# Performance work log

Hardware: AMD Instinct MI355X
Metric: run time of the kernel (lower is better)

## Reference

```python
import jax, jax.numpy as jnp
import numpy as np

NEG_SLOPE = 0.2  # PyG GATConv default negative_slope


def _gat_conv(h, src, dst, N, W, a_src, a_dst, b, heads):
    """PyG GATConv (eval mode, self-loops already in src/dst).
    h: [N, F_in], W: [F_in, heads*C], a_src/a_dst: [heads, C], b: [heads*C]."""
    C = W.shape[1] // heads
    hl = (h @ W).reshape(N, heads, C)                      # [N,H,C]
    al_s = jnp.einsum('nhc,hc->nh', hl, a_src)             # [N,H]
    al_d = jnp.einsum('nhc,hc->nh', hl, a_dst)             # [N,H]
    e = jax.nn.leaky_relu(al_s[src] + al_d[dst], NEG_SLOPE)  # [E,H]
    # segment softmax over incoming edges of each destination node
    m = jax.ops.segment_max(e, dst, num_segments=N)        # [N,H]
    ex = jnp.exp(e - m[dst])
    s = jax.ops.segment_sum(ex, dst, num_segments=N)
    alpha = ex / (s[dst] + 1e-16)                          # [E,H]
    out = jax.ops.segment_sum(hl[src] * alpha[:, :, None], dst, num_segments=N)
    return out.reshape(N, heads * C) + b


def setup_inputs() -> dict:
    key = jax.random.key(0)
    ks = jax.random.split(key, 16)
    N, E, D = 30000, 240000, 64
    NUM_ENT, NUM_REL, NUM_DRUGS = 100000, 64, 200
    sc = 0.1
    return {
        'x': jax.random.randint(ks[0], (N,), 0, NUM_ENT),
        'edge_index': jax.random.randint(ks[1], (2, E), 0, N),
        'edge_type': jax.random.randint(ks[2], (N,), 0, NUM_REL),
        'ent_emb': jax.random.normal(ks[3], (NUM_ENT, D), jnp.float32) * sc,
        'rel_emb': jax.random.normal(ks[4], (NUM_REL, D), jnp.float32) * sc,
        'W1': jax.random.normal(ks[5], (2 * D, 8 * D), jnp.float32) * sc,
        'att1_src': jax.random.normal(ks[6], (8, D), jnp.float32) * sc,
        'att1_dst': jax.random.normal(ks[7], (8, D), jnp.float32) * sc,
        'b1': jax.random.normal(ks[8], (8 * D,), jnp.float32) * sc,
        'W2': jax.random.normal(ks[9], (9 * D, D), jnp.float32) * sc,
        'att2_src': jax.random.normal(ks[10], (1, D), jnp.float32) * sc,
        'att2_dst': jax.random.normal(ks[11], (1, D), jnp.float32) * sc,
        'b2': jax.random.normal(ks[12], (D,), jnp.float32) * sc,
        'fc_w': jax.random.normal(ks[13], (D, NUM_DRUGS), jnp.float32) * sc,
        'fc_b': jax.random.normal(ks[14], (NUM_DRUGS,), jnp.float32) * sc,
    }


def reference(x, edge_index, edge_type, ent_emb, rel_emb, W1, att1_src, att1_dst, b1,
              W2, att2_src, att2_dst, b2, fc_w, fc_b):
    N = x.shape[0]
    loop = jnp.arange(N)
    src = jnp.concatenate([edge_index[0], loop])  # GATConv add_self_loops=True
    dst = jnp.concatenate([edge_index[1], loop])
    ent = ent_emb[x]                               # [N,D]
    rel = rel_emb[edge_type]                       # [N,D]
    h = jnp.concatenate([ent, rel], axis=-1)       # [N,2D]  (dropout is identity in eval)
    h = jax.nn.elu(_gat_conv(h, src, dst, N, W1, att1_src, att1_dst, b1, heads=8))  # [N,8D]
    h = jnp.concatenate([h, ent], axis=-1)         # [N,9D]
    h = jax.nn.elu(_gat_conv(h, src, dst, N, W2, att2_src, att2_dst, b2, heads=1))  # [N,D]
    g = jnp.mean(h, axis=0, keepdims=True)         # [1,D]
    return g @ fc_w + fc_b                         # [1,num_drugs]
```

## Files before the change

### kernel.cpp

```cpp
#include <hip/hip_runtime.h>
#include <math.h>

#define NEG_SLOPE 0.2f

typedef __attribute__((ext_vector_type(8))) short short8;
typedef __attribute__((ext_vector_type(4))) float f32x4;
typedef __attribute__((ext_vector_type(2))) float f32x2;

__device__ __forceinline__ float lrelu(float v) { return v > 0.f ? v : NEG_SLOPE * v; }
__device__ __forceinline__ float elu(float v) { return v > 0.f ? v : (__expf(v) - 1.f); }
__device__ __forceinline__ unsigned short f2b(float f) {
    unsigned u = __float_as_uint(f);
    return (unsigned short)((u + 0x7FFFu + ((u >> 16) & 1u)) >> 16);
}
__device__ __forceinline__ float blo(unsigned v) { return __uint_as_float(v << 16); }
__device__ __forceinline__ float bhi(unsigned v) { return __uint_as_float(v & 0xFFFF0000u); }
__device__ __forceinline__ unsigned packb(float a, float b) {
    return ((unsigned)f2b(b) << 16) | (unsigned)f2b(a);
}
__device__ __forceinline__ unsigned short pack8(float a, float b) {
    return (unsigned short)(__builtin_amdgcn_cvt_pk_fp8_f32(a, b, 0, false) & 0xFFFF);
}
__device__ __forceinline__ f32x2 unpack8(unsigned v) {
    return __builtin_amdgcn_cvt_pk_f32_fp8((int)v, false);
}
__device__ __forceinline__ f32x2 unpack8hi(unsigned v) {
    return __builtin_amdgcn_cvt_pk_f32_fp8((int)v, true);
}
__device__ __forceinline__ unsigned bpack_trunc(f32x2 f) {
    return (__float_as_uint(f.y) & 0xFFFF0000u) | (__float_as_uint(f.x) >> 16);
}
__device__ __forceinline__ int sw(int r, int o) { return (o ^ (r & 7)) << 3; }

__global__ __launch_bounds__(256) void init_k(int* __restrict__ zbase, int zwords,
                                              const float* __restrict__ W1,
                                              const float* __restrict__ W2,
                                              const float* __restrict__ a1s,
                                              const float* __restrict__ a1d,
                                              unsigned short* __restrict__ wsb,
                                              unsigned short* __restrict__ W1t,
                                              unsigned short* __restrict__ W2t) {
    int t = blockIdx.x * blockDim.x + threadIdx.x;
    int stride = gridDim.x * blockDim.x;
    for (int i = t; i < zwords; i += stride) zbase[i] = 0;
    for (int i = t; i < 2048; i += stride) {
        int hh = i >> 7, k = i & 127, h = hh & 7;
        const float* aw = (hh < 8) ? a1s : a1d;
        const float* wr = W1 + (size_t)k * 512 + h * 64;
        float s_ = 0.f;
#pragma unroll 16
        for (int c = 0; c < 64; c++) s_ += wr[c] * aw[h * 64 + c];
        wsb[i] = f2b(s_);
    }
    for (int i = t; i < 512 * 128; i += stride) {
        int n = i >> 7, kk = i & 127;
        W1t[i] = f2b(W1[(size_t)kk * 512 + n]);
    }
    for (int i = t; i < 64 * 576; i += stride) {
        int n = i / 576, k = i % 576;
        W2t[i] = f2b(W2[(size_t)k * 64 + n]);
    }
}

__global__ void prep_k(const int* __restrict__ x, const int* __restrict__ et,
                       const int* __restrict__ ei,
                       const float* __restrict__ ent_emb, const float* __restrict__ rel_emb,
                       unsigned* __restrict__ h1b2, unsigned short* __restrict__ h1q,
                       int* __restrict__ deg, int N, int E) {
    int t = blockIdx.x * blockDim.x + threadIdx.x;
    if (t < N * 64) {
        int n = t >> 6, j = t & 63;
        float v0, v1;
        if (j < 32) {
            const float* e = ent_emb + (size_t)x[n] * 64 + 2 * j;
            v0 = e[0]; v1 = e[1];
        } else {
            const float* r = rel_emb + (size_t)et[n] * 64 + 2 * (j - 32);
            v0 = r[0]; v1 = r[1];
        }
        h1b2[t] = packb(v0, v1);
        h1q[t] = pack8(v0, v1);
    }
    if (t < E + N) {
        int dst = t < E ? ei[E + t] : t - E;
        atomicAdd(&deg[dst], 1);
    }
}

__global__ __launch_bounds__(256) void attn1_k(const unsigned short* __restrict__ A,
                                               const unsigned short* __restrict__ Bt,
                                               float* __restrict__ als, float* __restrict__ ald,
                                               int M) {
    __shared__ __align__(16) unsigned short As[128 * 128];
    __shared__ __align__(16) unsigned short Bs[16 * 128];
    int tid = threadIdx.x;
    int m0 = blockIdx.x * 128;
    for (int c = tid; c < 2048; c += 256) {
        int r = c >> 4, o = c & 15;
        int gr = m0 + r;
        uint4 v = make_uint4(0u, 0u, 0u, 0u);
        if (gr < M) v = *(const uint4*)(A + (size_t)gr * 128 + o * 8);
        *(uint4*)(As + r * 128 + sw(r, o)) = v;
    }
    if (tid < 256) {
        int r = tid >> 4, o = tid & 15;
        uint4 v = *(const uint4*)(Bt + (size_t)r * 128 + o * 8);
        *(uint4*)(Bs + r * 128 + sw(r, o)) = v;
    }
    __syncthreads();
    int w = tid >> 6, lane = tid & 63;
    int wr = w * 32;
    int m16 = lane & 15, quad = lane >> 4;
    f32x4 acc[2] = {};
#pragma unroll
    for (int kk = 0; kk < 128; kk += 32) {
        int ob = (kk >> 3) + quad;
        short8 b = *(const short8*)(Bs + m16 * 128 + sw(m16, ob));
#pragma unroll
        for (int i = 0; i < 2; i++) {
            int r = wr + i * 16 + m16;
            short8 a = *(const short8*)(As + r * 128 + sw(r, ob));
            acc[i] = __builtin_amdgcn_mfma_f32_16x16x32_bf16(a, b, acc[i], 0, 0, 0);
        }
    }
#pragma unroll
    for (int i = 0; i < 2; i++)
#pragma unroll
        for (int reg = 0; reg < 4; reg++) {
            int row = m0 + wr + i * 16 + quad * 4 + reg;
            if (row < M) {
                if (m16 < 8) als[row * 8 + m16] = acc[i][reg];
                else         ald[row * 8 + (m16 - 8)] = acc[i][reg];
            }
        }
}

__global__ __launch_bounds__(256) void scan_k(const int* __restrict__ deg,
                                              int* __restrict__ offs,
                                              int* __restrict__ bstate,
                                              int N, int Etot, int NB) {
    __shared__ int s[256];
    __shared__ int sbase;
    int b = blockIdx.x, t = threadIdx.x;
    int i = b * 256 + t;
    int v = (i < N) ? deg[i] : 0;
    s[t] = v;
    __syncthreads();
    for (int off = 1; off < 256; off <<= 1) {
        int tmp = (t >= off) ? s[t - off] : 0;
        __syncthreads();
        s[t] += tmp;
        __syncthreads();
    }
    int total = s[255];
    if (t == 0) {
        if (b == 0) {
            atomicExch(&bstate[0], (total << 2) | 2);
            sbase = 0;
        } else {
            atomicExch(&bstate[b], (total << 2) | 1);
            int run = 0;
            for (int p = b - 1; p >= 0;) {
                int stv;
                do { stv = atomicAdd(&bstate[p], 0); } while ((stv & 3) == 0);
                run += (stv >> 2);
                if ((stv & 3) == 2) break;
                p--;
            }
            atomicExch(&bstate[b], ((run + total) << 2) | 2);
            sbase = run;
        }
    }
    __syncthreads();
    if (i < N) offs[i] = sbase + s[t] - v;
    if (b == NB - 1 && t == 0) offs[N] = Etot;
}

__global__ void fill_k(const int* __restrict__ ei, int E, int N,
                       const int* __restrict__ offs, int* __restrict__ cursor,
                       int* __restrict__ csr) {
    int e = blockIdx.x * blockDim.x + threadIdx.x;
    if (e >= E + N) return;
    int src = e < E ? ei[e] : e - E;
    int dst = e < E ? ei[E + e] : e - E;
    int pos = offs[dst] + atomicAdd(&cursor[dst], 1);
    csr[pos] = src;
}

__global__ __launch_bounds__(256) void alpha1_k(const float* __restrict__ als1,
                                                const float* __restrict__ ald1,
                                                const int* __restrict__ offs,
                                                const int* __restrict__ csr,
                                                float* __restrict__ ex1,
                                                float* __restrict__ inv1, int N) {
    int slot = threadIdx.x >> 3, h = threadIdx.x & 7;
    int n = blockIdx.x * 32 + slot;
    if (n >= N) return;
    float dl = ald1[n * 8 + h];
    int p0 = offs[n], p1 = offs[n + 1];
    float ssum = 0.f;
    for (int p = p0; p < p1; p++) {
        int src = csr[p];
        float xv = __expf(lrelu(als1[src * 8 + h] + dl));
        ex1[(size_t)p * 8 + h] = xv;
        ssum += xv;
    }
    inv1[n * 8 + h] = 8.f / (ssum + 1e-16f);
}

__global__ __launch_bounds__(256) void aggG_k(const unsigned short* __restrict__ h1q,
                                              const unsigned* __restrict__ h1b2,
                                              const float* __restrict__ ex1,
                                              const float* __restrict__ inv1,
                                              const int* __restrict__ offs,
                                              const int* __restrict__ csr,
                                              unsigned short* __restrict__ Gq,
                                              unsigned* __restrict__ h2u, int N) {
    int wv = threadIdx.x >> 6;
    int t = threadIdx.x & 63;
    int n = blockIdx.x * 4 + wv;
    if (n >= N) return;
    int p0 = offs[n], p1 = offs[n + 1];
    float a0[8] = {}, a1[8] = {};
    int p = p0;
    for (; p + 1 < p1; p += 2) {
        int sA = csr[p], sB = csr[p + 1];
        float4 eA0 = *(const float4*)(ex1 + (size_t)p * 8);
        float4 eA1 = *(const float4*)(ex1 + (size_t)p * 8 + 4);
        float4 eB0 = *(const float4*)(ex1 + (size_t)p * 8 + 8);
        float4 eB1 = *(const float4*)(ex1 + (size_t)p * 8 + 12);
        unsigned hA = h1q[sA * 64 + t];
        unsigned hB = h1q[sB * 64 + t];
        f32x2 fA = unpack8(hA), fB = unpack8(hB);
        float evA[8] = {eA0.x, eA0.y, eA0.z, eA0.w, eA1.x, eA1.y, eA1.z, eA1.w};
        float evB[8] = {eB0.x, eB0.y, eB0.z, eB0.w, eB1.x, eB1.y, eB1.z, eB1.w};
#pragma unroll
        for (int h = 0; h < 8; h++) {
            a0[h] += evA[h] * fA.x + evB[h] * fB.x;
            a1[h] += evA[h] * fA.y + evB[h] * fB.y;
        }
    }
    if (p < p1) {
        int sA = csr[p];
        float4 eA0 = *(const float4*)(ex1 + (size_t)p * 8);
        float4 eA1 = *(const float4*)(ex1 + (size_t)p * 8 + 4);
        f32x2 fA = unpack8(h1q[sA * 64 + t]);
        float evA[8] = {eA0.x, eA0.y, eA0.z, eA0.w, eA1.x, eA1.y, eA1.z, eA1.w};
#pragma unroll
        for (int h = 0; h < 8; h++) { a0[h] += evA[h] * fA.x; a1[h] += evA[h] * fA.y; }
    }
    float4 i0 = *(const float4*)(inv1 + n * 8);
    float4 i1 = *(const float4*)(inv1 + n * 8 + 4);
    float iv[8] = {i0.x, i0.y, i0.z, i0.w, i1.x, i1.y, i1.z, i1.w};
#pragma unroll
    for (int h = 0; h < 8; h++)
        Gq[(n * 8 + h) * 64 + t] = pack8(a0[h] * iv[h], a1[h] * iv[h]);
    if (t < 32)
        h2u[(size_t)n * 288 + 256 + t] = h1b2[n * 64 + t];
}

__global__ __launch_bounds__(256) void gemmG_k(const unsigned char* __restrict__ Gq8,
                                               const unsigned short* __restrict__ W1t,
                                               const float* __restrict__ b1,
                                               unsigned short* __restrict__ h2, int M) {
    __shared__ __align__(16) unsigned short As[128 * 128];
    __shared__ __align__(16) unsigned short Bs[64 * 128];
    int tid = threadIdx.x;
    int m0 = blockIdx.x * 128, h = blockIdx.y;
    for (int c = tid; c < 1024; c += 256) {
        int r = c >> 3, o = c & 7;
        int gr = m0 + r;
        uint4 v = make_uint4(0u, 0u, 0u, 0u);
        if (gr < M) v = *(const uint4*)(Gq8 + ((size_t)gr * 8 + h) * 128 + o * 16);
        uint4 w0, w1;
        w0.x = bpack_trunc(unpack8(v.x));   w0.y = bpack_trunc(unpack8hi(v.x));
        w0.z = bpack_trunc(unpack8(v.y));   w0.w = bpack_trunc(unpack8hi(v.y));
        w1.x = bpack_trunc(unpack8(v.z));   w1.y = bpack_trunc(unpack8hi(v.z));
        w1.z = bpack_trunc(unpack8(v.w));   w1.w = bpack_trunc(unpack8hi(v.w));
        *(uint4*)(As + r * 128 + sw(r, 2 * o)) = w0;
        *(uint4*)(As + r * 128 + sw(r, 2 * o + 1)) = w1;
    }
    for (int c = tid; c < 1024; c += 256) {
        int r = c >> 4, o = c & 15;
        uint4 v = *(const uint4*)(W1t + (size_t)(h * 64 + r) * 128 + o * 8);
        *(uint4*)(Bs + r * 128 + sw(r, o)) = v;
    }
    __syncthreads();
    int w = tid >> 6, lane = tid & 63;
    int wr = w * 32;
    int m16 = lane & 15, quad = lane >> 4;
    f32x4 acc[2][4] = {};
#pragma unroll
    for (int kk = 0; kk < 128; kk += 32) {
        int ob = (kk >> 3) + quad;
        short8 b[4];
#pragma unroll
        for (int j = 0; j < 4; j++) {
            int r = j * 16 + m16;
            b[j] = *(const short8*)(Bs + r * 128 + sw(r, ob));
        }
#pragma unroll
        for (int i = 0; i < 2; i++) {
            int r = wr + i * 16 + m16;
            short8 a = *(const short8*)(As + r * 128 + sw(r, ob));
#pragma unroll
            for (int j = 0; j < 4; j++)
                acc[i][j] = __builtin_amdgcn_mfma_f32_16x16x32_bf16(a, b[j], acc[i][j], 0, 0, 0);
        }
    }
#pragma unroll
    for (int i = 0; i < 2; i++)
#pragma unroll
        for (int j = 0; j < 4; j++)
#pragma unroll
            for (int reg = 0; reg < 4; reg++) {
                int row = m0 + wr + i * 16 + quad * 4 + reg;
                int col = h * 64 + j * 16 + m16;
                if (row < M)
                    h2[(size_t)row * 576 + col] = f2b(elu(acc[i][j][reg] * 0.125f + b1[col]));
            }
}

__global__ __launch_bounds__(256) void gemm2_k(const unsigned short* __restrict__ A,
                                               const unsigned short* __restrict__ Bt,
                                               const float* __restrict__ a2s,
                                               const float* __restrict__ a2d,
                                               unsigned char* __restrict__ hl2q,
                                               float* __restrict__ als2,
                                               float* __restrict__ ald2, int M) {
    __shared__ __align__(16) unsigned short As[64 * 64];
    __shared__ __align__(16) unsigned short Bs[64 * 64];
    int tid = threadIdx.x;
    int m0 = blockIdx.x * 64;
    int w = tid >> 6, lane = tid & 63;
    int m16 = lane & 15, quad = lane >> 4;
    f32x4 acc[4] = {};
    for (int k0 = 0; k0 < 576; k0 += 64) {
        __syncthreads();
        for (int c = tid; c < 512; c += 256) {
            int r = c >> 3, o = c & 7;
            int gr = m0 + r;
            uint4 v = make_uint4(0u, 0u, 0u, 0u);
            if (gr < M) v = *(const uint4*)(A + (size_t)gr * 576 + k0 + o * 8);
            *(uint4*)(As + r * 64 + sw(r, o)) = v;
        }
        for (int c = tid; c < 512; c += 256) {
            int r = c >> 3, o = c & 7;
            uint4 v = *(const uint4*)(Bt + (size_t)r * 576 + k0 + o * 8);
            *(uint4*)(Bs + r * 64 + sw(r, o)) = v;
        }
        __syncthreads();
#pragma unroll
        for (int kk = 0; kk < 64; kk += 32) {
            int ob = (kk >> 3) + quad;
            int r = w * 16 + m16;
            short8 a = *(const short8*)(As + r * 64 + sw(r, ob));
#pragma unroll
            for (int j = 0; j < 4; j++) {
                int rb = j * 16 + m16;
                short8 b = *(const short8*)(Bs + rb * 64 + sw(rb, ob));
                acc[j] = __builtin_amdgcn_mfma_f32_16x16x32_bf16(a, b, acc[j], 0, 0, 0);
            }
        }
    }
#pragma unroll
    for (int j = 0; j < 4; j++)
#pragma unroll
        for (int reg = 0; reg < 4; reg++) {
            int row = m0 + w * 16 + quad * 4 + reg;
            int col = j * 16 + m16;
            if (row < M)
                hl2q[(size_t)row * 64 + col] =
                    (unsigned char)(__builtin_amdgcn_cvt_pk_fp8_f32(acc[j][reg], 0.f, 0, false) & 0xFF);
        }
    float sa[4] = {}, sd[4] = {};
#pragma unroll
    for (int j = 0; j < 4; j++) {
        int col = j * 16 + m16;
        float as_ = a2s[col], ad_ = a2d[col];
#pragma unroll
        for (int reg = 0; reg < 4; reg++) {
            sa[reg] += acc[j][reg] * as_;
            sd[reg] += acc[j][reg] * ad_;
        }
    }
#pragma unroll
    for (int m = 1; m < 16; m <<= 1)
#pragma unroll
        for (int reg = 0; reg < 4; reg++) {
            sa[reg] += __shfl_xor(sa[reg], m, 64);
            sd[reg] += __shfl_xor(sd[reg], m, 64);
        }
    if (m16 == 0)
#pragma unroll
        for (int reg = 0; reg < 4; reg++) {
            int row = m0 + w * 16 + quad * 4 + reg;
            if (row < M) { als2[row] = sa[reg]; ald2[row] = sd[reg]; }
        }
}

__global__ __launch_bounds__(256) void agg2_k(const unsigned short* __restrict__ hl2q16,
                                              const float* __restrict__ als2,
                                              const float* __restrict__ ald2,
                                              const float* __restrict__ b2,
                                              const int* __restrict__ offs,
                                              const int* __restrict__ csr,
                                              float* __restrict__ gpart, int N) {
    __shared__ float red[512];
    int slot = threadIdx.x >> 5, l = threadIdx.x & 31;
    int n = blockIdx.x * 8 + slot;
    float v0 = 0.f, v1 = 0.f;
    if (n < N) {
        float dl = ald2[n];
        int p0 = offs[n], p1 = offs[n + 1];
        float a0 = 0.f, a1 = 0.f, ssum = 0.f;
        int p = p0;
        for (; p + 1 < p1; p += 2) {
            int sA = csr[p], sB = csr[p + 1];
            float lA = als2[sA], lB = als2[sB];
            unsigned hA = hl2q16[sA * 32 + l];
            unsigned hB = hl2q16[sB * 32 + l];
            float xA = __expf(lrelu(lA + dl));
            float xB = __expf(lrelu(lB + dl));
            ssum += xA + xB;
            f32x2 fA = unpack8(hA), fB = unpack8(hB);
            a0 += xA * fA.x + xB * fB.x;
            a1 += xA * fA.y + xB * fB.y;
        }
        if (p < p1) {
            int sA = csr[p];
            float xA = __expf(lrelu(als2[sA] + dl));
            ssum += xA;
            f32x2 fA = unpack8(hl2q16[sA * 32 + l]);
            a0 += xA * fA.x;
            a1 += xA * fA.y;
        }
        float inv = 1.f / (ssum + 1e-16f);
        v0 = elu(a0 * inv + b2[2 * l]);
        v1 = elu(a1 * inv + b2[2 * l + 1]);
    }
    red[slot * 64 + 2 * l] = v0;
    red[slot * 64 + 2 * l + 1] = v1;
    __syncthreads();
    if (threadIdx.x < 64) {
        float s = 0.f;
#pragma unroll
        for (int ss = 0; ss < 8; ss++) s += red[ss * 64 + threadIdx.x];
        gpart[(size_t)blockIdx.x * 64 + threadIdx.x] = s;
    }
}

__global__ __launch_bounds__(256) void colredfinal_k(const float* __restrict__ gpart,
                                                     float* __restrict__ gsum,
                                                     int* __restrict__ done,
                                                     const float* __restrict__ fcw,
                                                     const float* __restrict__ fcb,
                                                     float* __restrict__ out,
                                                     int NBL, int N, int NCB) {
    __shared__ float red[256];
    __shared__ int isLast;
    int t = threadIdx.x;
    int c = t & 63, rg = t >> 6;
    int bend = blockIdx.x * 256 + 256; if (bend > NBL) bend = NBL;
    float acc = 0.f;
    for (int b = blockIdx.x * 256 + rg; b < bend; b += 4)
        acc += gpart[(size_t)b * 64 + c];
    red[t] = acc;
    __syncthreads();
    if (t < 64) atomicAdd(&gsum[c], red[c] + red[c + 64] + red[c + 128] + red[c + 192]);
    __threadfence();
    if (t == 0) {
        int old = atomicAdd(done, 1);
        isLast = (old == NCB - 1) ? 1 : 0;
    }
    __syncthreads();
    if (isLast) {
        __shared__ float g[64];
        if (t < 64) g[t] = atomicAdd(&gsum[t], 0.f) / (float)N;
        __syncthreads();
        if (t < 200) {
            float a = fcb[t];
#pragma unroll
            for (int cc = 0; cc < 64; cc++) a += g[cc] * fcw[cc * 200 + t];
            out[t] = a;
        }
    }
}

extern "C" void kernel_launch(void* const* d_in, const int* in_sizes, int n_in,
                              void* d_out, int out_size, void* d_ws, size_t ws_size,
                              hipStream_t stream) {
    const int* x = (const int*)d_in[0];
    const int* ei = (const int*)d_in[1];
    const int* et = (const int*)d_in[2];
    const float* ent_emb = (const float*)d_in[3];
    const float* rel_emb = (const float*)d_in[4];
    const float* W1 = (const float*)d_in[5];
    const float* a1s = (const float*)d_in[6];
    const float* a1d = (const float*)d_in[7];
    const float* b1 = (const float*)d_in[8];
    const float* W2 = (const float*)d_in[9];
    const float* a2s = (const float*)d_in[10];
    const float* a2d = (const float*)d_in[11];
    const float* b2 = (const float*)d_in[12];
    const float* fcw = (const float*)d_in[13];
    const float* fcb = (const float*)d_in[14];
    float* out = (float*)d_out;

    int N = in_sizes[0];
    int E = in_sizes[1] / 2;
    int Etot = E + N;
    int NB = (N + 255) / 256;
    int NBL = (N + 7) / 8;
    int NCB = (NBL + 255) / 256;

    char* p = (char*)d_ws;
    auto alloc = [&](size_t bytes) -> char* {
        char* r = p;
        p += (bytes + 255) & ~(size_t)255;
        return r;
    };
    unsigned* h1b2 = (unsigned*)alloc((size_t)N * 64 * 4);
    unsigned short* h1q = (unsigned short*)alloc((size_t)N * 64 * 2);
    unsigned short* wsb = (unsigned short*)alloc(2048 * 2);
    unsigned short* W1t = (unsigned short*)alloc((size_t)512 * 128 * 2);
    unsigned short* W2t = (unsigned short*)alloc((size_t)64 * 576 * 2);
    float* als1 = (float*)alloc((size_t)N * 8 * 4);
    float* ald1 = (float*)alloc((size_t)N * 8 * 4);
    float* ex1  = (float*)alloc((size_t)Etot * 8 * 4);
    float* inv1 = (float*)alloc((size_t)N * 8 * 4);
    unsigned short* Gq = (unsigned short*)alloc((size_t)N * 512 * 2);
    unsigned short* h2  = (unsigned short*)alloc((size_t)N * 576 * 2);
    unsigned char* hl2q = (unsigned char*)alloc((size_t)N * 64);
    float* als2 = (float*)alloc((size_t)N * 4);
    float* ald2 = (float*)alloc((size_t)N * 4);
    float* gpart = (float*)alloc((size_t)NBL * 64 * 4);
    int* offs   = (int*)alloc((size_t)(N + 1) * 4);
    int* csr    = (int*)alloc((size_t)Etot * 4);
    char* z0 = p;
    int* deg    = (int*)alloc((size_t)N * 4);
    int* cursor = (int*)alloc((size_t)N * 4);
    float* gsum = (float*)alloc(64 * 4);
    int* done   = (int*)alloc(4);
    int* bstate = (int*)alloc((size_t)NB * 4);
    size_t zwords = (size_t)(p - z0) / 4;

    int tb = 256;
    init_k<<<256, tb, 0, stream>>>((int*)z0, (int)zwords, W1, W2, a1s, a1d, wsb, W1t, W2t);
    prep_k<<<(N * 64 + tb - 1) / tb, tb, 0, stream>>>(x, et, ei, ent_emb, rel_emb,
                                                      h1b2, h1q, deg, N, E);
    attn1_k<<<(N + 127) / 128, 256, 0, stream>>>((const unsigned short*)h1b2, wsb, als1, ald1, N);
    scan_k<<<NB, 256, 0, stream>>>(deg, offs, bstate, N, Etot, NB);
    fill_k<<<(Etot + tb - 1) / tb, tb, 0, stream>>>(ei, E, N, offs, cursor, csr);
    alpha1_k<<<(N + 31) / 32, 256, 0, stream>>>(als1, ald1, offs, csr, ex1, inv1, N);
    aggG_k<<<(N + 3) / 4, 256, 0, stream>>>(h1q, h1b2, ex1, inv1, offs, csr, Gq, (unsigned*)h2, N);
    gemmG_k<<<dim3((N + 127) / 128, 8), 256, 0, stream>>>((const unsigned char*)Gq, W1t, b1, h2, N);
    gemm2_k<<<(N + 63) / 64, 256, 0, stream>>>(h2, W2t, a2s, a2d, hl2q, als2, ald2, N);
    agg2_k<<<NBL, 256, 0, stream>>>((const unsigned short*)hl2q, als2, ald2, b2, offs, csr, gpart, N);
    colredfinal_k<<<NCB, 256, 0, stream>>>(gpart, gsum, done, fcw, fcb, out, NBL, N, NCB);
}
```

Before: 269.7 us.

## Store layer-2 input in fp8, fold init into prep, unroll aggregation by four

The intermediate h2 buffer (N x 576) is now written as fp8 instead of bf16, and gemm2 converts fp8 to bf16 while staging into shared memory, halving that buffer's traffic. The init kernel is removed: zeroing uses hipMemsetAsync and the weight transposes and attention-weight folding move into prep_k. The aggG edge loop is unrolled from 2 to 4 edges for more memory-level parallelism, and the ent columns copied into h2 now come from the fp8 h1q copy. Storing in fp8 loses precision in the second GAT layer input.

```diff
diff --git a/kernel.cpp b/kernel.cpp
--- a/kernel.cpp
+++ b/kernel.cpp
@@ -32,41 +32,15 @@
 }
 __device__ __forceinline__ int sw(int r, int o) { return (o ^ (r & 7)) << 3; }
 
-__global__ __launch_bounds__(256) void init_k(int* __restrict__ zbase, int zwords,
-                                              const float* __restrict__ W1,
-                                              const float* __restrict__ W2,
-                                              const float* __restrict__ a1s,
-                                              const float* __restrict__ a1d,
-                                              unsigned short* __restrict__ wsb,
-                                              unsigned short* __restrict__ W1t,
-                                              unsigned short* __restrict__ W2t) {
-    int t = blockIdx.x * blockDim.x + threadIdx.x;
-    int stride = gridDim.x * blockDim.x;
-    for (int i = t; i < zwords; i += stride) zbase[i] = 0;
-    for (int i = t; i < 2048; i += stride) {
-        int hh = i >> 7, k = i & 127, h = hh & 7;
-        const float* aw = (hh < 8) ? a1s : a1d;
-        const float* wr = W1 + (size_t)k * 512 + h * 64;
-        float s_ = 0.f;
-#pragma unroll 16
-        for (int c = 0; c < 64; c++) s_ += wr[c] * aw[h * 64 + c];
-        wsb[i] = f2b(s_);
-    }
-    for (int i = t; i < 512 * 128; i += stride) {
-        int n = i >> 7, kk = i & 127;
-        W1t[i] = f2b(W1[(size_t)kk * 512 + n]);
-    }
-    for (int i = t; i < 64 * 576; i += stride) {
-        int n = i / 576, k = i % 576;
-        W2t[i] = f2b(W2[(size_t)k * 64 + n]);
-    }
-}
-
 __global__ void prep_k(const int* __restrict__ x, const int* __restrict__ et,
                        const int* __restrict__ ei,
                        const float* __restrict__ ent_emb, const float* __restrict__ rel_emb,
+                       const float* __restrict__ W1, const float* __restrict__ W2,
+                       const float* __restrict__ a1s, const float* __restrict__ a1d,
                        unsigned* __restrict__ h1b2, unsigned short* __restrict__ h1q,
-                       int* __restrict__ deg, int N, int E) {
+                       unsigned short* __restrict__ wsb, unsigned short* __restrict__ W1t,
+                       unsigned short* __restrict__ W2t, int* __restrict__ deg,
+                       int N, int E) {
     int t = blockIdx.x * blockDim.x + threadIdx.x;
     if (t < N * 64) {
         int n = t >> 6, j = t & 63;
@@ -80,6 +54,23 @@
         }
         h1b2[t] = packb(v0, v1);
         h1q[t] = pack8(v0, v1);
+    }
+    if (t < 2048) {
+        int hh = t >> 7, k = t & 127, h = hh & 7;
+        const float* aw = (hh < 8) ? a1s : a1d;
+        const float* wr = W1 + (size_t)k * 512 + h * 64;
+        float s_ = 0.f;
+#pragma unroll 16
+        for (int c = 0; c < 64; c++) s_ += wr[c] * aw[h * 64 + c];
+        wsb[t] = f2b(s_);
+    }
+    if (t < 512 * 128) {
+        int n = t >> 7, kk = t & 127;
+        W1t[t] = f2b(W1[(size_t)kk * 512 + n]);
+    }
+    if (t < 64 * 576) {
+        int n = t / 576, k = t % 576;
+        W2t[t] = f2b(W2[(size_t)k * 64 + n]);
     }
     if (t < E + N) {
         int dst = t < E ? ei[E + t] : t - E;
@@ -209,13 +200,12 @@
 }
 
 __global__ __launch_bounds__(256) void aggG_k(const unsigned short* __restrict__ h1q,
-                                              const unsigned* __restrict__ h1b2,
                                               const float* __restrict__ ex1,
                                               const float* __restrict__ inv1,
                                               const int* __restrict__ offs,
                                               const int* __restrict__ csr,
                                               unsigned short* __restrict__ Gq,
-                                              unsigned* __restrict__ h2u, int N) {
+                                              unsigned short* __restrict__ h2q16, int N) {
     int wv = threadIdx.x >> 6;
     int t = threadIdx.x & 63;
     int n = blockIdx.x * 4 + wv;
@@ -223,24 +213,32 @@
     int p0 = offs[n], p1 = offs[n + 1];
     float a0[8] = {}, a1[8] = {};
     int p = p0;
-    for (; p + 1 < p1; p += 2) {
-        int sA = csr[p], sB = csr[p + 1];
+    for (; p + 3 < p1; p += 4) {
+        int sA = csr[p], sB = csr[p + 1], sC = csr[p + 2], sD = csr[p + 3];
         float4 eA0 = *(const float4*)(ex1 + (size_t)p * 8);
         float4 eA1 = *(const float4*)(ex1 + (size_t)p * 8 + 4);
         float4 eB0 = *(const float4*)(ex1 + (size_t)p * 8 + 8);
         float4 eB1 = *(const float4*)(ex1 + (size_t)p * 8 + 12);
+        float4 eC0 = *(const float4*)(ex1 + (size_t)p * 8 + 16);
+        float4 eC1 = *(const float4*)(ex1 + (size_t)p * 8 + 20);
+        float4 eD0 = *(const float4*)(ex1 + (size_t)p * 8 + 24);
+        float4 eD1 = *(const float4*)(ex1 + (size_t)p * 8 + 28);
         unsigned hA = h1q[sA * 64 + t];
         unsigned hB = h1q[sB * 64 + t];
-        f32x2 fA = unpack8(hA), fB = unpack8(hB);
+        unsigned hC = h1q[sC * 64 + t];
+        unsigned hD = h1q[sD * 64 + t];
+        f32x2 fA = unpack8(hA), fB = unpack8(hB), fC = unpack8(hC), fD = unpack8(hD);
         float evA[8] = {eA0.x, eA0.y, eA0.z, eA0.w, eA1.x, eA1.y, eA1.z, eA1.w};
         float evB[8] = {eB0.x, eB0.y, eB0.z, eB0.w, eB1.x, eB1.y, eB1.z, eB1.w};
+        float evC[8] = {eC0.x, eC0.y, eC0.z, eC0.w, eC1.x, eC1.y, eC1.z, eC1.w};
+        float evD[8] = {eD0.x, eD0.y, eD0.z, eD0.w, eD1.x, eD1.y, eD1.z, eD1.w};
 #pragma unroll
         for (int h = 0; h < 8; h++) {
-            a0[h] += evA[h] * fA.x + evB[h] * fB.x;
-            a1[h] += evA[h] * fA.y + evB[h] * fB.y;
-        }
-    }
-    if (p < p1) {
+            a0[h] += evA[h] * fA.x + evB[h] * fB.x + evC[h] * fC.x + evD[h] * fD.x;
+            a1[h] += evA[h] * fA.y + evB[h] * fB.y + evC[h] * fC.y + evD[h] * fD.y;
+        }
+    }
+    for (; p < p1; p++) {
         int sA = csr[p];
         float4 eA0 = *(const float4*)(ex1 + (size_t)p * 8);
         float4 eA1 = *(const float4*)(ex1 + (size_t)p * 8 + 4);
@@ -256,13 +254,13 @@
     for (int h = 0; h < 8; h++)
         Gq[(n * 8 + h) * 64 + t] = pack8(a0[h] * iv[h], a1[h] * iv[h]);
     if (t < 32)
-        h2u[(size_t)n * 288 + 256 + t] = h1b2[n * 64 + t];
+        h2q16[(size_t)n * 288 + 256 + t] = h1q[n * 64 + t];
 }
 
 __global__ __launch_bounds__(256) void gemmG_k(const unsigned char* __restrict__ Gq8,
                                                const unsigned short* __restrict__ W1t,
                                                const float* __restrict__ b1,
-                                               unsigned short* __restrict__ h2, int M) {
+                                               unsigned char* __restrict__ h2q8, int M) {
     __shared__ __align__(16) unsigned short As[128 * 128];
     __shared__ __align__(16) unsigned short Bs[64 * 128];
     int tid = threadIdx.x;
@@ -316,12 +314,15 @@
             for (int reg = 0; reg < 4; reg++) {
                 int row = m0 + wr + i * 16 + quad * 4 + reg;
                 int col = h * 64 + j * 16 + m16;
-                if (row < M)
-                    h2[(size_t)row * 576 + col] = f2b(elu(acc[i][j][reg] * 0.125f + b1[col]));
+                if (row < M) {
+                    float v = elu(acc[i][j][reg] * 0.125f + b1[col]);
+                    h2q8[(size_t)row * 576 + col] =
+                        (unsigned char)(__builtin_amdgcn_cvt_pk_fp8_f32(v, 0.f, 0, false) & 0xFF);
+                }
             }
 }
 
-__global__ __launch_bounds__(256) void gemm2_k(const unsigned short* __restrict__ A,
+__global__ __launch_bounds__(256) void gemm2_k(const unsigned char* __restrict__ Aq8,
                                                const unsigned short* __restrict__ Bt,
                                                const float* __restrict__ a2s,
                                                const float* __restrict__ a2d,
@@ -337,12 +338,18 @@
     f32x4 acc[4] = {};
     for (int k0 = 0; k0 < 576; k0 += 64) {
         __syncthreads();
-        for (int c = tid; c < 512; c += 256) {
-            int r = c >> 3, o = c & 7;
+        {
+            int r = tid >> 2, o = tid & 3;
             int gr = m0 + r;
             uint4 v = make_uint4(0u, 0u, 0u, 0u);
-            if (gr < M) v = *(const uint4*)(A + (size_t)gr * 576 + k0 + o * 8);
-            *(uint4*)(As + r * 64 + sw(r, o)) = v;
+            if (gr < M) v = *(const uint4*)(Aq8 + (size_t)gr * 576 + k0 + o * 16);
+            uint4 w0, w1;
+            w0.x = bpack_trunc(unpack8(v.x));   w0.y = bpack_trunc(unpack8hi(v.x));
+            w0.z = bpack_trunc(unpack8(v.y));   w0.w = bpack_trunc(unpack8hi(v.y));
+            w1.x = bpack_trunc(unpack8(v.z));   w1.y = bpack_trunc(unpack8hi(v.z));
+            w1.z = bpack_trunc(unpack8(v.w));   w1.w = bpack_trunc(unpack8hi(v.w));
+            *(uint4*)(As + r * 64 + sw(r, 2 * o)) = w0;
+            *(uint4*)(As + r * 64 + sw(r, 2 * o + 1)) = w1;
         }
         for (int c = tid; c < 512; c += 256) {
             int r = c >> 3, o = c & 7;
@@ -530,7 +537,7 @@
     float* ex1  = (float*)alloc((size_t)Etot * 8 * 4);
     float* inv1 = (float*)alloc((size_t)N * 8 * 4);
     unsigned short* Gq = (unsigned short*)alloc((size_t)N * 512 * 2);
-    unsigned short* h2  = (unsigned short*)alloc((size_t)N * 576 * 2);
+    unsigned char* h2q8 = (unsigned char*)alloc((size_t)N * 576);
     unsigned char* hl2q = (unsigned char*)alloc((size_t)N * 64);
     float* als2 = (float*)alloc((size_t)N * 4);
     float* ald2 = (float*)alloc((size_t)N * 4);
@@ -543,19 +550,22 @@
     float* gsum = (float*)alloc(64 * 4);
     int* done   = (int*)alloc(4);
     int* bstate = (int*)alloc((size_t)NB * 4);
-    size_t zwords = (size_t)(p - z0) / 4;
+    size_t zbytes = (size_t)(p - z0);
 
     int tb = 256;
-    init_k<<<256, tb, 0, stream>>>((int*)z0, (int)zwords, W1, W2, a1s, a1d, wsb, W1t, W2t);
+    hipMemsetAsync(z0, 0, zbytes, stream);
     prep_k<<<(N * 64 + tb - 1) / tb, tb, 0, stream>>>(x, et, ei, ent_emb, rel_emb,
-                                                      h1b2, h1q, deg, N, E);
+                                                      W1, W2, a1s, a1d, h1b2, h1q,
+                                                      wsb, W1t, W2t, deg, N, E);
     attn1_k<<<(N + 127) / 128, 256, 0, stream>>>((const unsigned short*)h1b2, wsb, als1, ald1, N);
     scan_k<<<NB, 256, 0, stream>>>(deg, offs, bstate, N, Etot, NB);
     fill_k<<<(Etot + tb - 1) / tb, tb, 0, stream>>>(ei, E, N, offs, cursor, csr);
     alpha1_k<<<(N + 31) / 32, 256, 0, stream>>>(als1, ald1, offs, csr, ex1, inv1, N);
-    aggG_k<<<(N + 3) / 4, 256, 0, stream>>>(h1q, h1b2, ex1, inv1, offs, csr, Gq, (unsigned*)h2, N);
-    gemmG_k<<<dim3((N + 127) / 128, 8), 256, 0, stream>>>((const unsigned char*)Gq, W1t, b1, h2, N);
-    gemm2_k<<<(N + 63) / 64, 256, 0, stream>>>(h2, W2t, a2s, a2d, hl2q, als2, ald2, N);
+    aggG_k<<<(N + 3) / 4, 256, 0, stream>>>(h1q, ex1, inv1, offs, csr, Gq,
+                                            (unsigned short*)h2q8, N);
+    gemmG_k<<<dim3((N + 127) / 128, 8), 256, 0, stream>>>((const unsigned char*)Gq, W1t, b1,
+                                                          h2q8, N);
+    gemm2_k<<<(N + 63) / 64, 256, 0, stream>>>(h2q8, W2t, a2s, a2d, hl2q, als2, ald2, N);
     agg2_k<<<NBL, 256, 0, stream>>>((const unsigned short*)hl2q, als2, ald2, b2, offs, csr, gpart, N);
     colredfinal_k<<<NCB, 256, 0, stream>>>(gpart, gsum, done, fcw, fcb, out, NBL, N, NCB);
 }
```

After: 263.9 us (median of 2 runs). 1.02x faster.
